# Optimization experiments

Measured on AMD Instinct MI355X. Metric: run time of the kernel, lower is better.

The kernel has to match this reference:

```python
import jax, jax.numpy as jnp
import numpy as np

N = 100000   # nodes
E = 1600000  # edges
IN = 128     # input_dim
H = 64       # hidden_dim
C = 10       # num_classes
L = 4        # num_layers
G = 200      # graphs in batch
BN_EPS = 1e-5


def setup_inputs() -> dict:
    key = jax.random.key(0)
    ks = jax.random.split(key, 12)
    s = 0.05
    h = jax.random.normal(ks[0], (N, IN), jnp.float32)
    snorm_n = jax.random.uniform(ks[1], (N, 1), jnp.float32)
    src = jax.random.randint(ks[2], (E,), 0, N, jnp.int32)
    dst = jax.random.randint(ks[3], (E,), 0, N, jnp.int32)
    graph_ids = jnp.sort(jax.random.randint(ks[4], (N,), 0, G, jnp.int32))
    W_embed = jax.random.normal(ks[5], (IN, H), jnp.float32) * s
    b_embed = jnp.zeros((H,), jnp.float32)
    eps = jnp.zeros((L,), jnp.float32)               # learnable eps, init 0
    W1 = jax.random.normal(ks[6], (L, H, H), jnp.float32) * s
    b1 = jnp.zeros((L, H), jnp.float32)
    g1 = jnp.ones((L, H), jnp.float32)               # MLP-internal BN gamma
    be1 = jnp.zeros((L, H), jnp.float32)             # MLP-internal BN beta
    W2 = jax.random.normal(ks[7], (L, H, H), jnp.float32) * s
    b2 = jnp.zeros((L, H), jnp.float32)
    g2 = jnp.ones((L, H), jnp.float32)               # bn_node_h gamma
    be2 = jnp.zeros((L, H), jnp.float32)             # bn_node_h beta
    Wlin = jax.random.normal(ks[8], (L + 1, H, C), jnp.float32) * s
    blin = jnp.zeros((L + 1, C), jnp.float32)
    return dict(h=h, snorm_n=snorm_n, src=src, dst=dst, graph_ids=graph_ids,
                W_embed=W_embed, b_embed=b_embed, eps=eps,
                W1=W1, b1=b1, g1=g1, be1=be1, W2=W2, b2=b2, g2=g2, be2=be2,
                Wlin=Wlin, blin=blin)


def _batchnorm(x, gamma, beta):
    # training-mode BatchNorm1d over the node axis
    m = jnp.mean(x, axis=0)
    v = jnp.mean(jnp.square(x - m), axis=0)
    return gamma * (x - m) * jax.lax.rsqrt(v + BN_EPS) + beta


def reference(h, snorm_n, src, dst, graph_ids, W_embed, b_embed, eps,
              W1, b1, g1, be1, W2, b2, g2, be2, Wlin, blin):
    # node embedding
    h = h @ W_embed + b_embed                                   # [N, H]
    hidden_rep = [h]
    for i in range(L):
        h_in = h
        # copy_u + sum reduce: neigh[v] = sum_{(u->v)} h[u]
        neigh = jax.ops.segment_sum(h[src], dst, num_segments=N)  # [N, H]
        h = (1.0 + eps[i]) * h + neigh
        # apply_func: 2-layer MLP with internal BN+ReLU (standard GIN MLP)
        h = jax.nn.relu(_batchnorm(h @ W1[i] + b1[i], g1[i], be1[i]))
        h = h @ W2[i] + b2[i]
        h = h * snorm_n                                          # graph_norm
        h = _batchnorm(h, g2[i], be2[i])                         # bn_node_h
        h = jax.nn.relu(h)
        h = h_in + h                                             # residual
        # dropout p=0.0 -> identity
        hidden_rep.append(h)
    score = jnp.zeros((G, C), h.dtype)
    for i, hr in enumerate(hidden_rep):
        pooled = jax.ops.segment_sum(hr, graph_ids, num_segments=G)  # SumPooling
        score = score + pooled @ Wlin[i] + blin[i]
    return score
```

## Files before the change

kernel.cpp:

```cpp
#include <hip/hip_runtime.h>
#include <hip/hip_bf16.h>
#include <math.h>

#define NN 100000
#define NE 1600000
#define KIN 128
#define HD 64
#define NC 10
#define NL 4
#define NG 200
#define NBKT 196

typedef short s16x8 __attribute__((ext_vector_type(8)));
typedef float f32x4 __attribute__((ext_vector_type(4)));
using f4 = float4;

static __device__ __forceinline__ ushort f2bf(float x) {
  __hip_bfloat16 b = __float2bfloat16(x);
  return *reinterpret_cast<ushort*>(&b);
}
static __device__ __forceinline__ float bf2f(ushort u) {
  return __uint_as_float(((unsigned)u) << 16);
}
static __device__ __forceinline__ s16x8 zero8() {
  s16x8 v;
#pragma unroll
  for (int i = 0; i < 8; ++i) v[i] = 0;
  return v;
}

__global__ __launch_bounds__(256) void bucket_hist(const int* __restrict__ dst,
                                                   int* __restrict__ gbucket) {
  __shared__ int lh[NBKT];
  int tid = threadIdx.x;
  for (int i = tid; i < NBKT; i += 256) lh[i] = 0;
  __syncthreads();
  int base = blockIdx.x * 4096;
#pragma unroll 4
  for (int it = 0; it < 16; ++it) {
    int e = base + it * 256 + tid;
    if (e < NE) atomicAdd(&lh[dst[e] >> 9], 1);
  }
  __syncthreads();
  for (int i = tid; i < NBKT; i += 256)
    if (lh[i]) atomicAdd(&gbucket[i], lh[i]);
}

__global__ __launch_bounds__(256) void bucket_scan(const int* __restrict__ gbucket,
                                                   int* __restrict__ bbase,
                                                   int* __restrict__ bcur) {
  __shared__ int s[256];
  int tid = threadIdx.x;
  int v = (tid < NBKT) ? gbucket[tid] : 0;
  s[tid] = v;
  __syncthreads();
  for (int off = 1; off < 256; off <<= 1) {
    int t = (tid >= off) ? s[tid - off] : 0;
    __syncthreads();
    s[tid] += t;
    __syncthreads();
  }
  int excl = s[tid] - v;
  if (tid <= NBKT) bbase[tid] = excl;
  if (tid < NBKT) bcur[tid] = excl;
}

__global__ __launch_bounds__(256) void bucket_scatter(const int* __restrict__ src,
                                                      const int* __restrict__ dst,
                                                      int* __restrict__ bcur,
                                                      int2* __restrict__ pairs) {
  __shared__ int lh[NBKT];
  __shared__ int lbase[NBKT];
  int tid = threadIdx.x;
  for (int i = tid; i < NBKT; i += 256) lh[i] = 0;
  __syncthreads();
  int base = blockIdx.x * 4096;
  int dloc[16], sloc[16];
#pragma unroll
  for (int it = 0; it < 16; ++it) {
    int e = base + it * 256 + tid;
    bool ok = e < NE;
    dloc[it] = ok ? dst[e] : -1;
    sloc[it] = ok ? src[e] : 0;
    if (ok) atomicAdd(&lh[dloc[it] >> 9], 1);
  }
  __syncthreads();
  for (int i = tid; i < NBKT; i += 256) {
    int c = lh[i];
    lbase[i] = c ? atomicAdd(&bcur[i], c) : 0;
    lh[i] = 0;
  }
  __syncthreads();
#pragma unroll
  for (int it = 0; it < 16; ++it) {
    int d = dloc[it];
    if (d >= 0) {
      int b = d >> 9;
      int p = lbase[b] + atomicAdd(&lh[b], 1);
      pairs[p] = make_int2(d, sloc[it]);
    }
  }
}

__global__ __launch_bounds__(256) void csr_build(const int2* __restrict__ pairs,
                                                 const int* __restrict__ bbase,
                                                 int* __restrict__ row_ptr,
                                                 int* __restrict__ csr_src) {
  __shared__ int deg[512];
  __shared__ int psum[256];
  __shared__ int cur[512];
  int b = blockIdx.x;
  int tid = threadIdx.x;
  int beg = bbase[b], end = bbase[b + 1];
  int node0 = b << 9;
  deg[tid] = 0;
  deg[tid + 256] = 0;
  __syncthreads();
  for (int i = beg + tid; i < end; i += 256)
    atomicAdd(&deg[pairs[i].x - node0], 1);
  __syncthreads();
  int a0 = deg[2 * tid], a1 = deg[2 * tid + 1];
  psum[tid] = a0 + a1;
  __syncthreads();
  for (int off = 1; off < 256; off <<= 1) {
    int t = (tid >= off) ? psum[tid - off] : 0;
    __syncthreads();
    psum[tid] += t;
    __syncthreads();
  }
  int pe = psum[tid] - (a0 + a1);
  int e0 = pe, e1 = pe + a0;
  cur[2 * tid] = e0;
  cur[2 * tid + 1] = e1;
  int n0 = node0 + 2 * tid, n1 = node0 + 2 * tid + 1;
  if (n0 < NN) row_ptr[n0] = beg + e0;
  if (n1 < NN) row_ptr[n1] = beg + e1;
  __syncthreads();
  for (int i = beg + tid; i < end; i += 256) {
    int2 pr = pairs[i];
    int p = atomicAdd(&cur[pr.x - node0], 1);
    csr_src[beg + p] = pr.y;
  }
  if (b == 0 && tid == 0) row_ptr[NN] = NE;
}

__global__ __launch_bounds__(256) void gstart_kernel(const int* __restrict__ gid,
                                                     int* __restrict__ gstart) {
  int g = threadIdx.x + blockIdx.x * 256;
  if (g > NG) return;
  int lo = 0, hi = NN;
  while (lo < hi) {
    int mid = (lo + hi) >> 1;
    if (gid[mid] < g)
      lo = mid + 1;
    else
      hi = mid;
  }
  gstart[g] = lo;
}

__global__ __launch_bounds__(256) void pack_weights(
    const float* __restrict__ Wemb, const float* __restrict__ W1,
    const float* __restrict__ W2, ushort* __restrict__ Wpk) {
  int t = blockIdx.x;
  const float* src = (t < 2)   ? Wemb + t * 4096
                     : (t < 6) ? W1 + (t - 2) * 4096
                               : W2 + (t - 6) * 4096;
  for (int idx = threadIdx.x; idx < 4096; idx += 256) {
    int k = idx >> 6, n = idx & 63;
    int dsti = ((k >> 5) * 4 + (n >> 4)) * 512 +
               (((k >> 3) & 3) * 16 + (n & 15)) * 8 + (k & 7);
    Wpk[t * 4096 + dsti] = f2bf(src[idx]);
  }
}

__global__ __launch_bounds__(256) void pool_kernel(const float* __restrict__ h,
                                                   const int* __restrict__ gid,
                                                   float* __restrict__ pooledL) {
  int tid = threadIdx.x;
  int c = tid & 63;
  int rg = tid >> 6;
  int r0 = blockIdx.x * 128;
  int rend = r0 + 128 < NN ? r0 + 128 : NN;
  int rstart = r0 + rg;
  int cur = gid[rstart < NN ? rstart : NN - 1];
  float acc = 0.f;
  for (int r = rstart; r < rend; r += 4) {
    int g = gid[r];
    if (g != cur) {
      atomicAdd(&pooledL[cur * HD + c], acc);
      acc = 0.f;
      cur = g;
    }
    acc += h[r * HD + c];
  }
  atomicAdd(&pooledL[cur * HD + c], acc);
}

__global__ __launch_bounds__(256) void gather_kernel(
    const float* __restrict__ h, const ushort* __restrict__ hbf,
    const int* __restrict__ rp, const int* __restrict__ csrc,
    const float* __restrict__ eps_p, ushort* __restrict__ aggbf) {
  int node = blockIdx.x * 32 + (threadIdx.x >> 3);
  int lane = threadIdx.x & 7;
  if (node >= NN) return;
  int beg = rp[node], end = rp[node + 1];
  float epsv = 1.0f + eps_p[0];
  f4 sa = *reinterpret_cast<const f4*>(&h[node * HD + lane * 8]);
  f4 sb = *reinterpret_cast<const f4*>(&h[node * HD + lane * 8 + 4]);
  float acc[8] = {epsv * sa.x, epsv * sa.y, epsv * sa.z, epsv * sa.w,
                  epsv * sb.x, epsv * sb.y, epsv * sb.z, epsv * sb.w};
  int e = beg;
  for (; e + 1 < end; e += 2) {
    int s0 = csrc[e], s1 = csrc[e + 1];
    f4 v0 = *reinterpret_cast<const f4*>(&hbf[s0 * HD + lane * 8]);
    f4 v1 = *reinterpret_cast<const f4*>(&hbf[s1 * HD + lane * 8]);
    const ushort* u0 = reinterpret_cast<const ushort*>(&v0);
    const ushort* u1 = reinterpret_cast<const ushort*>(&v1);
#pragma unroll
    for (int j = 0; j < 8; ++j) acc[j] += bf2f(u0[j]) + bf2f(u1[j]);
  }
  if (e < end) {
    int s0 = csrc[e];
    f4 v0 = *reinterpret_cast<const f4*>(&hbf[s0 * HD + lane * 8]);
    const ushort* u0 = reinterpret_cast<const ushort*>(&v0);
#pragma unroll
    for (int j = 0; j < 8; ++j) acc[j] += bf2f(u0[j]);
  }
  alignas(16) ushort us[8];
#pragma unroll
  for (int j = 0; j < 8; ++j) us[j] = f2bf(acc[j]);
  *reinterpret_cast<s16x8*>(&aggbf[(size_t)node * HD + lane * 8]) =
      *reinterpret_cast<const s16x8*>(us);
}

template <int MODE>
__global__ __launch_bounds__(256, 4) void gemm_kernel(
    const void* Xin, const ushort* __restrict__ wt,
    const float* __restrict__ bias, const float* __restrict__ bn_in,
    const float* __restrict__ g1p, const float* __restrict__ be1p,
    const float* __restrict__ snorm, float* out, float* __restrict__ bn_out,
    ushort* __restrict__ hbf) {
  __shared__ ushort lds_a[128 * 64];
  __shared__ ushort lds_b[4096];
  __shared__ float lds_red[2][4][64];
  __shared__ float lds_bn[2][64];

  const int tid = threadIdx.x;
  const int row0 = blockIdx.x * 128;
  const int w = tid >> 6;
  const int l = tid & 63;
  const int lr = l >> 4, lc = l & 15;

  if (MODE == 2) {
    if (tid < 64) {
      float s = bn_in[tid], q = bn_in[64 + tid];
      float m = s * (1.0f / NN);
      float r = rsqrtf(q * (1.0f / NN) - m * m + 1e-5f);
      float scl = g1p[tid] * r;
      lds_bn[0][tid] = scl;
      lds_bn[1][tid] = be1p[tid] - m * scl;
    }
    __syncthreads();
  }

  f32x4 acc[2][4];
#pragma unroll
  for (int mi = 0; mi < 2; ++mi)
#pragma unroll
    for (int nf = 0; nf < 4; ++nf)
#pragma unroll
      for (int r = 0; r < 4; ++r) acc[mi][nf][r] = 0.f;

  const int KT = (MODE == 0) ? 2 : 1;
  for (int kt = 0; kt < KT; ++kt) {
    if (kt) __syncthreads();
#pragma unroll
    for (int i = 0; i < 2; ++i) {
      int ch = i * 256 + tid;
      *reinterpret_cast<s16x8*>(&lds_b[ch * 8]) =
          *reinterpret_cast<const s16x8*>(&wt[kt * 4096 + ch * 8]);
    }
#pragma unroll
    for (int i = 0; i < 4; ++i) {
      int f8i = i * 256 + tid;
      int row = f8i >> 3, c8 = f8i & 7;
      int grow = row0 + row;
      s16x8 val = zero8();
      if (grow < NN) {
        if (MODE == 1) {
          val = *reinterpret_cast<const s16x8*>(
              reinterpret_cast<const ushort*>(Xin) + (size_t)grow * HD + c8 * 8);
        } else {
          const float* p =
              (MODE == 0)
                  ? reinterpret_cast<const float*>(Xin) + (size_t)grow * KIN + kt * 64 + c8 * 8
                  : reinterpret_cast<const float*>(Xin) + (size_t)grow * HD + c8 * 8;
          f4 x0 = *reinterpret_cast<const f4*>(p);
          f4 x1 = *reinterpret_cast<const f4*>(p + 4);
          float xv[8] = {x0.x, x0.y, x0.z, x0.w, x1.x, x1.y, x1.z, x1.w};
          if (MODE == 2) {
#pragma unroll
            for (int j = 0; j < 8; ++j) {
              int c = c8 * 8 + j;
              float v = xv[j] * lds_bn[0][c] + lds_bn[1][c];
              xv[j] = v > 0.f ? v : 0.f;
            }
          }
          alignas(16) ushort us[8];
#pragma unroll
          for (int j = 0; j < 8; ++j) us[j] = f2bf(xv[j]);
          val = *reinterpret_cast<const s16x8*>(us);
        }
      }
      int slot = c8 ^ (row & 7);
      *reinterpret_cast<s16x8*>(&lds_a[row * 64 + slot * 8]) = val;
    }
    __syncthreads();

    s16x8 af[2][2];
#pragma unroll
    for (int mi = 0; mi < 2; ++mi)
#pragma unroll
      for (int kh = 0; kh < 2; ++kh) {
        int row = w * 32 + mi * 16 + lc;
        int slot = (kh * 4 + lr) ^ (row & 7);
        af[mi][kh] = *reinterpret_cast<const s16x8*>(&lds_a[row * 64 + slot * 8]);
      }
#pragma unroll
    for (int kh = 0; kh < 2; ++kh)
#pragma unroll
      for (int nf = 0; nf < 4; ++nf) {
        s16x8 bf = *reinterpret_cast<const s16x8*>(&lds_b[(kh * 4 + nf) * 512 + l * 8]);
#pragma unroll
        for (int mi = 0; mi < 2; ++mi)
          acc[mi][nf] = __builtin_amdgcn_mfma_f32_16x16x32_bf16(
              af[mi][kh], bf, acc[mi][nf], 0, 0, 0);
      }
  }

  float bias_l[4];
#pragma unroll
  for (int nf = 0; nf < 4; ++nf) bias_l[nf] = bias[nf * 16 + lc];

  float psum[4] = {0.f, 0.f, 0.f, 0.f}, psq[4] = {0.f, 0.f, 0.f, 0.f};
#pragma unroll
  for (int mi = 0; mi < 2; ++mi)
#pragma unroll
    for (int r = 0; r < 4; ++r) {
      int grow = row0 + w * 32 + mi * 16 + lr * 4 + r;
      if (grow < NN) {
        float sn = (MODE == 2) ? snorm[grow] : 1.0f;
#pragma unroll
        for (int nf = 0; nf < 4; ++nf) {
          float v = acc[mi][nf][r] + bias_l[nf];
          if (MODE == 2) v *= sn;
          out[(size_t)grow * HD + nf * 16 + lc] = v;
          if (MODE == 0) {
            hbf[(size_t)grow * HD + nf * 16 + lc] = f2bf(v);
          } else {
            psum[nf] += v;
            psq[nf] += v * v;
          }
        }
      }
    }
  if (MODE != 0) {
#pragma unroll
    for (int nf = 0; nf < 4; ++nf) {
      psum[nf] += __shfl_xor(psum[nf], 16);
      psq[nf] += __shfl_xor(psq[nf], 16);
      psum[nf] += __shfl_xor(psum[nf], 32);
      psq[nf] += __shfl_xor(psq[nf], 32);
    }
    if (l < 16) {
#pragma unroll
      for (int nf = 0; nf < 4; ++nf) {
        lds_red[0][w][nf * 16 + l] = psum[nf];
        lds_red[1][w][nf * 16 + l] = psq[nf];
      }
    }
    __syncthreads();
    if (tid < 64) {
      float s = 0.f, q = 0.f;
#pragma unroll
      for (int w2 = 0; w2 < 4; ++w2) {
        s += lds_red[0][w2][tid];
        q += lds_red[1][w2][tid];
      }
      atomicAdd(&bn_out[tid], s);
      atomicAdd(&bn_out[64 + tid], q);
    }
  }
}

__global__ __launch_bounds__(256) void final_kernel(
    const float* __restrict__ t2, float* __restrict__ h,
    ushort* __restrict__ hbf, const float* __restrict__ g2p,
    const float* __restrict__ be2p, const float* __restrict__ stats2) {
  __shared__ float sc[64], sh[64];
  int tid = threadIdx.x;
  if (tid < 64) {
    float s = stats2[tid], q = stats2[64 + tid];
    float m = s * (1.0f / NN);
    float r = rsqrtf(q * (1.0f / NN) - m * m + 1e-5f);
    float scl = g2p[tid] * r;
    sc[tid] = scl;
    sh[tid] = be2p[tid] - m * scl;
  }
  __syncthreads();
  int idx = blockIdx.x * 256 + tid;
  int r = idx >> 3;
  int c0 = (idx & 7) * 8;
  f4 ta = *reinterpret_cast<const f4*>(&t2[r * HD + c0]);
  f4 tb = *reinterpret_cast<const f4*>(&t2[r * HD + c0 + 4]);
  f4 ha = *reinterpret_cast<const f4*>(&h[r * HD + c0]);
  f4 hb = *reinterpret_cast<const f4*>(&h[r * HD + c0 + 4]);
  float tt[8] = {ta.x, ta.y, ta.z, ta.w, tb.x, tb.y, tb.z, tb.w};
  float hh[8] = {ha.x, ha.y, ha.z, ha.w, hb.x, hb.y, hb.z, hb.w};
  float vals[8];
#pragma unroll
  for (int j = 0; j < 8; ++j) {
    int c = c0 + j;
    float v = tt[j] * sc[c] + sh[c];
    v = v > 0.f ? v : 0.f;
    vals[j] = hh[j] + v;
  }
  *reinterpret_cast<f4*>(&h[r * HD + c0]) =
      make_float4(vals[0], vals[1], vals[2], vals[3]);
  *reinterpret_cast<f4*>(&h[r * HD + c0 + 4]) =
      make_float4(vals[4], vals[5], vals[6], vals[7]);
  alignas(16) ushort us[8];
#pragma unroll
  for (int j = 0; j < 8; ++j) us[j] = f2bf(vals[j]);
  *reinterpret_cast<s16x8*>(&hbf[r * HD + c0]) =
      *reinterpret_cast<const s16x8*>(us);
}

__global__ __launch_bounds__(256) void score_kernel(
    const float* __restrict__ pooled, const float* __restrict__ Wlin,
    const float* __restrict__ blin, float* __restrict__ out) {
  int o = blockIdx.x * 256 + threadIdx.x;
  if (o >= NG * NC) return;
  int g = o / NC, c = o % NC;
  float s = 0.f;
  for (int i = 0; i <= NL; ++i) {
    s += blin[i * NC + c];
    const float* pg = &pooled[i * NG * HD + g * HD];
    const float* wl = &Wlin[i * HD * NC + c];
    float acc = 0.f;
#pragma unroll 8
    for (int k = 0; k < HD; ++k) acc += pg[k] * wl[k * NC];
    s += acc;
  }
  out[o] = s;
}

extern "C" void kernel_launch(void* const* d_in, const int* in_sizes, int n_in,
                              void* d_out, int out_size, void* d_ws,
                              size_t ws_size, hipStream_t stream) {
  const float* X = (const float*)d_in[0];
  const float* snorm = (const float*)d_in[1];
  const int* src = (const int*)d_in[2];
  const int* dst = (const int*)d_in[3];
  const int* gid = (const int*)d_in[4];
  const float* W_embed = (const float*)d_in[5];
  const float* b_embed = (const float*)d_in[6];
  const float* eps = (const float*)d_in[7];
  const float* W1 = (const float*)d_in[8];
  const float* b1 = (const float*)d_in[9];
  const float* g1 = (const float*)d_in[10];
  const float* be1 = (const float*)d_in[11];
  const float* W2 = (const float*)d_in[12];
  const float* b2 = (const float*)d_in[13];
  const float* g2 = (const float*)d_in[14];
  const float* be2 = (const float*)d_in[15];
  const float* Wlin = (const float*)d_in[16];
  const float* blin = (const float*)d_in[17];

  float* ws = (float*)d_ws;
  float* h_buf = ws;
  float* t1 = h_buf + (size_t)NN * HD;
  float* pooled = t1 + (size_t)NN * HD;
  float* stats = pooled + 5 * NG * HD;
  int* ib = (int*)(stats + NL * 256);
  int* row_ptr = ib;
  int* gstart = ib + 100004;
  int* gbucket = ib + 100208;
  int* bbase = ib + 100404;
  int* bcur = ib + 100604;
  int* csr_src = ib + 100800;
  ushort* h_bf = (ushort*)(ib + 100800 + NE);
  ushort* agg_bf = h_bf + (size_t)NN * HD;
  ushort* Wpk = agg_bf + (size_t)NN * HD;
  int2* pairs = (int2*)t1;

  const int GEMM_GRID = (NN + 127) / 128;
  const int EBLK = (NE + 4095) / 4096;
  const int POOL_GRID = (NN + 127) / 128;

  hipMemsetAsync(pooled, 0, (5 * NG * HD + NL * 256) * sizeof(float), stream);
  hipMemsetAsync(gbucket, 0, NBKT * sizeof(int), stream);

  pack_weights<<<10, 256, 0, stream>>>(W_embed, W1, W2, Wpk);

  bucket_hist<<<EBLK, 256, 0, stream>>>(dst, gbucket);
  bucket_scan<<<1, 256, 0, stream>>>(gbucket, bbase, bcur);
  bucket_scatter<<<EBLK, 256, 0, stream>>>(src, dst, bcur, pairs);
  csr_build<<<NBKT, 256, 0, stream>>>(pairs, bbase, row_ptr, csr_src);
  gstart_kernel<<<1, 256, 0, stream>>>(gid, gstart);

  gemm_kernel<0><<<GEMM_GRID, 256, 0, stream>>>(
      X, Wpk, b_embed, nullptr, nullptr, nullptr, nullptr, h_buf, nullptr,
      h_bf);
  pool_kernel<<<POOL_GRID, 256, 0, stream>>>(h_buf, gid, pooled);

  for (int l = 0; l < NL; ++l) {
    float* st1 = stats + l * 256;
    float* st2 = stats + l * 256 + 128;
    gather_kernel<<<(NN + 31) / 32, 256, 0, stream>>>(h_buf, h_bf, row_ptr,
                                                      csr_src, eps + l, agg_bf);
    gemm_kernel<1><<<GEMM_GRID, 256, 0, stream>>>(
        agg_bf, Wpk + (2 + l) * 4096, b1 + l * 64, nullptr, nullptr, nullptr,
        nullptr, t1, st1, nullptr);
    gemm_kernel<2><<<GEMM_GRID, 256, 0, stream>>>(
        t1, Wpk + (6 + l) * 4096, b2 + l * 64, st1, g1 + l * 64, be1 + l * 64,
        snorm, t1, st2, nullptr);
    final_kernel<<<(NN * 8) / 256, 256, 0, stream>>>(
        t1, h_buf, h_bf, g2 + l * 64, be2 + l * 64, st2);
    pool_kernel<<<POOL_GRID, 256, 0, stream>>>(h_buf, gid,
                                               pooled + (l + 1) * NG * HD);
  }

  score_kernel<<<(NG * NC + 255) / 256, 256, 0, stream>>>(pooled, Wlin, blin,
                                                          (float*)d_out);
}
```

Measured before the change: 589.7 us.

## Fuse final BN/residual with sum pooling, unroll gather by four, drop unused gstart

```diff
diff --git a/kernel.cpp b/kernel.cpp
--- a/kernel.cpp
+++ b/kernel.cpp
@@ -142,21 +142,6 @@
     csr_src[beg + p] = pr.y;
   }
   if (b == 0 && tid == 0) row_ptr[NN] = NE;
-}
-
-__global__ __launch_bounds__(256) void gstart_kernel(const int* __restrict__ gid,
-                                                     int* __restrict__ gstart) {
-  int g = threadIdx.x + blockIdx.x * 256;
-  if (g > NG) return;
-  int lo = 0, hi = NN;
-  while (lo < hi) {
-    int mid = (lo + hi) >> 1;
-    if (gid[mid] < g)
-      lo = mid + 1;
-    else
-      hi = mid;
-  }
-  gstart[g] = lo;
 }
 
 __global__ __launch_bounds__(256) void pack_weights(
@@ -206,26 +191,27 @@
   if (node >= NN) return;
   int beg = rp[node], end = rp[node + 1];
   float epsv = 1.0f + eps_p[0];
-  f4 sa = *reinterpret_cast<const f4*>(&h[node * HD + lane * 8]);
-  f4 sb = *reinterpret_cast<const f4*>(&h[node * HD + lane * 8 + 4]);
+  f4 sa = *reinterpret_cast<const f4*>(&h[(size_t)node * HD + lane * 8]);
+  f4 sb = *reinterpret_cast<const f4*>(&h[(size_t)node * HD + lane * 8 + 4]);
   float acc[8] = {epsv * sa.x, epsv * sa.y, epsv * sa.z, epsv * sa.w,
                   epsv * sb.x, epsv * sb.y, epsv * sb.z, epsv * sb.w};
   int e = beg;
-  for (; e + 1 < end; e += 2) {
-    int s0 = csrc[e], s1 = csrc[e + 1];
-    f4 v0 = *reinterpret_cast<const f4*>(&hbf[s0 * HD + lane * 8]);
-    f4 v1 = *reinterpret_cast<const f4*>(&hbf[s1 * HD + lane * 8]);
-    const ushort* u0 = reinterpret_cast<const ushort*>(&v0);
-    const ushort* u1 = reinterpret_cast<const ushort*>(&v1);
-#pragma unroll
-    for (int j = 0; j < 8; ++j) acc[j] += bf2f(u0[j]) + bf2f(u1[j]);
-  }
-  if (e < end) {
+  for (; e + 4 <= end; e += 4) {
+    int s0 = csrc[e], s1 = csrc[e + 1], s2 = csrc[e + 2], s3 = csrc[e + 3];
+    s16x8 v0 = *reinterpret_cast<const s16x8*>(&hbf[(size_t)s0 * HD + lane * 8]);
+    s16x8 v1 = *reinterpret_cast<const s16x8*>(&hbf[(size_t)s1 * HD + lane * 8]);
+    s16x8 v2 = *reinterpret_cast<const s16x8*>(&hbf[(size_t)s2 * HD + lane * 8]);
+    s16x8 v3 = *reinterpret_cast<const s16x8*>(&hbf[(size_t)s3 * HD + lane * 8]);
+#pragma unroll
+    for (int j = 0; j < 8; ++j)
+      acc[j] += (bf2f((ushort)v0[j]) + bf2f((ushort)v1[j])) +
+                (bf2f((ushort)v2[j]) + bf2f((ushort)v3[j]));
+  }
+  for (; e < end; ++e) {
     int s0 = csrc[e];
-    f4 v0 = *reinterpret_cast<const f4*>(&hbf[s0 * HD + lane * 8]);
-    const ushort* u0 = reinterpret_cast<const ushort*>(&v0);
-#pragma unroll
-    for (int j = 0; j < 8; ++j) acc[j] += bf2f(u0[j]);
+    s16x8 v0 = *reinterpret_cast<const s16x8*>(&hbf[(size_t)s0 * HD + lane * 8]);
+#pragma unroll
+    for (int j = 0; j < 8; ++j) acc[j] += bf2f((ushort)v0[j]);
   }
   alignas(16) ushort us[8];
 #pragma unroll
@@ -394,47 +380,39 @@
   }
 }
 
-__global__ __launch_bounds__(256) void final_kernel(
+__global__ __launch_bounds__(256) void final_pool_kernel(
     const float* __restrict__ t2, float* __restrict__ h,
     ushort* __restrict__ hbf, const float* __restrict__ g2p,
-    const float* __restrict__ be2p, const float* __restrict__ stats2) {
-  __shared__ float sc[64], sh[64];
+    const float* __restrict__ be2p, const float* __restrict__ stats2,
+    const int* __restrict__ gid, float* __restrict__ pooledL) {
   int tid = threadIdx.x;
-  if (tid < 64) {
-    float s = stats2[tid], q = stats2[64 + tid];
-    float m = s * (1.0f / NN);
-    float r = rsqrtf(q * (1.0f / NN) - m * m + 1e-5f);
-    float scl = g2p[tid] * r;
-    sc[tid] = scl;
-    sh[tid] = be2p[tid] - m * scl;
-  }
-  __syncthreads();
-  int idx = blockIdx.x * 256 + tid;
-  int r = idx >> 3;
-  int c0 = (idx & 7) * 8;
-  f4 ta = *reinterpret_cast<const f4*>(&t2[r * HD + c0]);
-  f4 tb = *reinterpret_cast<const f4*>(&t2[r * HD + c0 + 4]);
-  f4 ha = *reinterpret_cast<const f4*>(&h[r * HD + c0]);
-  f4 hb = *reinterpret_cast<const f4*>(&h[r * HD + c0 + 4]);
-  float tt[8] = {ta.x, ta.y, ta.z, ta.w, tb.x, tb.y, tb.z, tb.w};
-  float hh[8] = {ha.x, ha.y, ha.z, ha.w, hb.x, hb.y, hb.z, hb.w};
-  float vals[8];
-#pragma unroll
-  for (int j = 0; j < 8; ++j) {
-    int c = c0 + j;
-    float v = tt[j] * sc[c] + sh[c];
+  int c = tid & 63;
+  int rg = tid >> 6;
+  float s = stats2[c], q = stats2[64 + c];
+  float m = s * (1.0f / NN);
+  float rr = rsqrtf(q * (1.0f / NN) - m * m + 1e-5f);
+  float scl = g2p[c] * rr;
+  float shv = be2p[c] - m * scl;
+  int r0 = blockIdx.x * 128;
+  int rend = r0 + 128 < NN ? r0 + 128 : NN;
+  int rstart = r0 + rg;
+  int cur = gid[rstart < NN ? rstart : NN - 1];
+  float pacc = 0.f;
+  for (int r = rstart; r < rend; r += 4) {
+    int g = gid[r];
+    if (g != cur) {
+      atomicAdd(&pooledL[cur * HD + c], pacc);
+      pacc = 0.f;
+      cur = g;
+    }
+    float v = t2[(size_t)r * HD + c] * scl + shv;
     v = v > 0.f ? v : 0.f;
-    vals[j] = hh[j] + v;
-  }
-  *reinterpret_cast<f4*>(&h[r * HD + c0]) =
-      make_float4(vals[0], vals[1], vals[2], vals[3]);
-  *reinterpret_cast<f4*>(&h[r * HD + c0 + 4]) =
-      make_float4(vals[4], vals[5], vals[6], vals[7]);
-  alignas(16) ushort us[8];
-#pragma unroll
-  for (int j = 0; j < 8; ++j) us[j] = f2bf(vals[j]);
-  *reinterpret_cast<s16x8*>(&hbf[r * HD + c0]) =
-      *reinterpret_cast<const s16x8*>(us);
+    float nv = h[(size_t)r * HD + c] + v;
+    h[(size_t)r * HD + c] = nv;
+    hbf[(size_t)r * HD + c] = f2bf(nv);
+    pacc += nv;
+  }
+  atomicAdd(&pooledL[cur * HD + c], pacc);
 }
 
 __global__ __launch_bounds__(256) void score_kernel(
@@ -485,12 +463,11 @@
   float* stats = pooled + 5 * NG * HD;
   int* ib = (int*)(stats + NL * 256);
   int* row_ptr = ib;
-  int* gstart = ib + 100004;
-  int* gbucket = ib + 100208;
-  int* bbase = ib + 100404;
-  int* bcur = ib + 100604;
-  int* csr_src = ib + 100800;
-  ushort* h_bf = (ushort*)(ib + 100800 + NE);
+  int* gbucket = ib + 100004;
+  int* bbase = ib + 100200;
+  int* bcur = ib + 100400;
+  int* csr_src = ib + 100600;
+  ushort* h_bf = (ushort*)(ib + 100600 + NE);
   ushort* agg_bf = h_bf + (size_t)NN * HD;
   ushort* Wpk = agg_bf + (size_t)NN * HD;
   int2* pairs = (int2*)t1;
@@ -508,7 +485,6 @@
   bucket_scan<<<1, 256, 0, stream>>>(gbucket, bbase, bcur);
   bucket_scatter<<<EBLK, 256, 0, stream>>>(src, dst, bcur, pairs);
   csr_build<<<NBKT, 256, 0, stream>>>(pairs, bbase, row_ptr, csr_src);
-  gstart_kernel<<<1, 256, 0, stream>>>(gid, gstart);
 
   gemm_kernel<0><<<GEMM_GRID, 256, 0, stream>>>(
       X, Wpk, b_embed, nullptr, nullptr, nullptr, nullptr, h_buf, nullptr,
@@ -526,10 +502,9 @@
     gemm_kernel<2><<<GEMM_GRID, 256, 0, stream>>>(
         t1, Wpk + (6 + l) * 4096, b2 + l * 64, st1, g1 + l * 64, be1 + l * 64,
         snorm, t1, st2, nullptr);
-    final_kernel<<<(NN * 8) / 256, 256, 0, stream>>>(
-        t1, h_buf, h_bf, g2 + l * 64, be2 + l * 64, st2);
-    pool_kernel<<<POOL_GRID, 256, 0, stream>>>(h_buf, gid,
-                                               pooled + (l + 1) * NG * HD);
+    final_pool_kernel<<<POOL_GRID, 256, 0, stream>>>(
+        t1, h_buf, h_bf, g2 + l * 64, be2 + l * 64, st2, gid,
+        pooled + (l + 1) * NG * HD);
   }
 
   score_kernel<<<(NG * NC + 255) / 256, 256, 0, stream>>>(pooled, Wlin, blin,
```

After: 639.0 us. +8.4%, slower.
